# Performance work log

Measured on AMD Instinct MI355X. Metric: run time of the kernel, lower is better.

## Reference

```python
import jax, jax.numpy as jnp
import numpy as np

N_NODES = 100000
N_EDGES = 1600000
HIDDEN = 64
NUM_GRAPHS = 512


def setup_inputs() -> dict:
    key = jax.random.key(0)
    k1, k2, k3, k4, k5, k6 = jax.random.split(key, 6)
    x = jax.random.normal(k1, (N_NODES, HIDDEN), dtype=jnp.float32)
    edge_index = jax.random.randint(k2, (2, N_EDGES), 0, N_NODES, dtype=jnp.int64)
    batch = jnp.sort(jax.random.randint(k3, (N_NODES,), 0, NUM_GRAPHS, dtype=jnp.int64))
    # SAGPooling's internal GraphConv(64 -> 1): lin_rel (with bias) on aggregated
    # neighbor features, lin_root (no bias) on self features.
    s = 1.0 / np.sqrt(HIDDEN)
    W_rel = jax.random.uniform(k4, (HIDDEN, 1), dtype=jnp.float32, minval=-s, maxval=s)
    b_rel = jax.random.uniform(k5, (1,), dtype=jnp.float32, minval=-s, maxval=s)
    W_root = jax.random.uniform(k6, (HIDDEN, 1), dtype=jnp.float32, minval=-s, maxval=s)
    return {"x": x, "edge_index": edge_index, "batch": batch,
            "W_rel": W_rel, "b_rel": b_rel, "W_root": W_root}


def reference(x, edge_index, batch, W_rel, b_rel, W_root):
    n = x.shape[0]
    src, dst = edge_index[0], edge_index[1]
    # GraphConv (aggr='add'): sum x_j over in-edges, then lin_rel(aggr)+lin_root(x)
    aggr = jax.ops.segment_sum(x[src], dst, num_segments=n)          # [N, H]
    score = (aggr @ W_rel + b_rel + x @ W_root)[:, 0]                # [N]
    # min_score=-1 -> scores softmax-normalized per graph; all nodes kept in order
    m = jax.ops.segment_max(score, batch, num_segments=NUM_GRAPHS)   # [G]
    e = jnp.exp(score - m[batch])
    z = jax.ops.segment_sum(e, batch, num_segments=NUM_GRAPHS)       # [G]
    att = e / z[batch]                                               # [N]
    att_x = x * att[:, None]                                         # [N, H]
    # global_add_pool
    return jax.ops.segment_sum(att_x, batch, num_segments=NUM_GRAPHS)  # [G, H]
```

## Files before the change

kernel.cpp:

```cpp
#include <hip/hip_runtime.h>
#include <math.h>
#include <stdint.h>


#define H 64
#define TILE 4096
#define NTHR_S 1024
#define EPT (TILE / NTHR_S)
#define BUCKET_SZ 256
#define MAX_NB 400
#define CAP 5120
#define ROWS_PER_WAVE 32
#define PSCALE 16384.0f
#define INV_PSCALE 6.103515625e-05f

__global__ __launch_bounds__(256) void node_prep(
    const float4* __restrict__ x4, const float4* __restrict__ W_rel4,
    const float4* __restrict__ W_root4,
    float* __restrict__ p, float* __restrict__ r,
    float* __restrict__ num, float* __restrict__ z,
    unsigned int* __restrict__ cursor,
    int n_nodes, int num_elems, int n_graphs, int nb)
{
    int gid = (int)(blockIdx.x * blockDim.x + threadIdx.x);
    if (gid < num_elems) num[gid] = 0.0f;
    else if (gid < num_elems + n_graphs) z[gid - num_elems] = 0.0f;
    else if (gid < num_elems + n_graphs + nb)
        cursor[gid - num_elems - n_graphs] =
            (unsigned int)(gid - num_elems - n_graphs) * CAP;

    int node = blockIdx.x * 64 + (threadIdx.x >> 2);
    int q    = threadIdx.x & 3;
    if (node >= n_nodes) return;

    float pv = 0.0f, rv = 0.0f;
    #pragma unroll
    for (int kk = 0; kk < 4; ++kk) {
        float4 v  = x4[node * 16 + kk * 4 + q];
        float4 wr = W_rel4[kk * 4 + q];
        float4 wo = W_root4[kk * 4 + q];
        pv += v.x * wr.x + v.y * wr.y + v.z * wr.z + v.w * wr.w;
        rv += v.x * wo.x + v.y * wo.y + v.z * wo.z + v.w * wo.w;
    }
    pv += __shfl_xor(pv, 1, 64); pv += __shfl_xor(pv, 2, 64);
    rv += __shfl_xor(rv, 1, 64); rv += __shfl_xor(rv, 2, 64);
    if (q == 0) { p[node] = pv; r[node] = rv; }
}

__global__ __launch_bounds__(NTHR_S) void edge_sort(
    const int* __restrict__ src, const int* __restrict__ dst,
    const float* __restrict__ p,
    unsigned int* __restrict__ cursor, unsigned int* __restrict__ sorted_g,
    int n_edges, int nb)
{
    __shared__ unsigned int hist[MAX_NB];
    __shared__ unsigned int offs[MAX_NB];
    __shared__ unsigned int gbase[MAX_NB];
    __shared__ unsigned int wtot[8];
    __shared__ unsigned int svals[TILE];
    __shared__ unsigned short sbid[TILE];

    int b = blockIdx.x;
    int base = b * TILE;
    int tile_n = min(TILE, n_edges - base);
    int tid = threadIdx.x;

    if (tid < nb) hist[tid] = 0;
    __syncthreads();

    unsigned int dd[EPT]; int ss[EPT];
    float pv[EPT];
    unsigned int bk[EPT], pk[EPT], slot[EPT];

    int j0 = tid * EPT;
    if (j0 + EPT <= tile_n) {
        int4 s4 = *(const int4*)(src + base + j0);
        int4 d4 = *(const int4*)(dst + base + j0);
        ss[0] = s4.x; ss[1] = s4.y; ss[2] = s4.z; ss[3] = s4.w;
        dd[0] = (unsigned int)d4.x; dd[1] = (unsigned int)d4.y;
        dd[2] = (unsigned int)d4.z; dd[3] = (unsigned int)d4.w;
    } else {
        #pragma unroll
        for (int u = 0; u < EPT; ++u) {
            int j = j0 + u;
            if (j < tile_n) { ss[u] = src[base + j];
                              dd[u] = (unsigned int)dst[base + j]; }
            else dd[u] = 0xFFFFFFFFu;
        }
    }
    #pragma unroll
    for (int u = 0; u < EPT; ++u)
        if (dd[u] != 0xFFFFFFFFu) pv[u] = p[ss[u]];
    #pragma unroll
    for (int u = 0; u < EPT; ++u) {
        if (dd[u] != 0xFFFFFFFFu) {
            bk[u] = dd[u] >> 8;
            int q = (int)__float2int_rn(pv[u] * PSCALE);
            q = max(-8388607, min(8388607, q));
            pk[u] = ((unsigned int)q << 8) | (dd[u] & 255u);
            slot[u] = atomicAdd(&hist[bk[u]], 1u);
        }
    }
    __syncthreads();

    int wv = tid >> 6, ln = tid & 63;
    unsigned int v = 0, xs = 0;
    if (wv < 7) {
        int bin = wv * 64 + ln;
        v = (bin < nb) ? hist[bin] : 0;
        xs = v;
        #pragma unroll
        for (int off = 1; off < 64; off <<= 1) {
            unsigned int y = __shfl_up(xs, off, 64);
            if (ln >= off) xs += y;
        }
        if (ln == 63) wtot[wv] = xs;
    }
    __syncthreads();
    if (wv < 7) {
        int bin = wv * 64 + ln;
        unsigned int pre = 0;
        #pragma unroll
        for (int w2 = 0; w2 < 7; ++w2)
            pre += (w2 < wv) ? wtot[w2] : 0u;
        if (bin < nb) {
            offs[bin]  = pre + xs - v;
            gbase[bin] = v ? atomicAdd(&cursor[bin], v) : 0u;
        }
    }
    __syncthreads();

    #pragma unroll
    for (int u = 0; u < EPT; ++u) {
        if (dd[u] != 0xFFFFFFFFu) {
            unsigned int pos = offs[bk[u]] + slot[u];
            svals[pos] = pk[u];
            sbid[pos]  = (unsigned short)bk[u];
        }
    }
    __syncthreads();

    for (int j = tid; j < tile_n; j += NTHR_S) {
        unsigned int bb = sbid[j];
        unsigned int gi = gbase[bb] + ((unsigned int)j - offs[bb]);
        if (gi < (bb + 1) * (unsigned int)CAP)
            sorted_g[gi] = svals[j];
    }
}

__global__ __launch_bounds__(256) void bucket_accum(
    const unsigned int* __restrict__ sorted_g,
    const unsigned int* __restrict__ cursor,
    const float* __restrict__ r,
    float* __restrict__ e_buf, int n_nodes)
{
    __shared__ int acc[BUCKET_SZ];
    int k = blockIdx.x;
    int tid = threadIdx.x;
    acc[tid] = 0;
    __syncthreads();

    unsigned int beg = (unsigned int)k * CAP;
    unsigned int cnt = min(cursor[k] - beg, (unsigned int)CAP);
    unsigned int n4  = cnt & ~3u;
    for (unsigned int j = tid * 4; j < n4; j += 1024) {
        uint4 v = *(const uint4*)(sorted_g + beg + j);
        atomicAdd(&acc[v.x & 255u], (int)v.x >> 8);
        atomicAdd(&acc[v.y & 255u], (int)v.y >> 8);
        atomicAdd(&acc[v.z & 255u], (int)v.z >> 8);
        atomicAdd(&acc[v.w & 255u], (int)v.w >> 8);
    }
    for (unsigned int j = n4 + tid; j < cnt; j += 256) {
        unsigned int v = sorted_g[beg + j];
        atomicAdd(&acc[v & 255u], (int)v >> 8);
    }
    __syncthreads();

    int node = k * BUCKET_SZ + tid;
    if (node < n_nodes)
        e_buf[node] = __expf((float)acc[tid] * INV_PSCALE + r[node]);
}

__global__ __launch_bounds__(256) void pool(
    const float* __restrict__ x, const float* __restrict__ e_buf,
    const int* __restrict__ batch,
    float* __restrict__ num, float* __restrict__ z, int n_nodes)
{
    int wid = threadIdx.x >> 6, lane = threadIdx.x & 63;
    int row0 = (blockIdx.x * 4 + wid) * ROWS_PER_WAVE;
    if (row0 >= n_nodes) return;
    int rend = min(row0 + ROWS_PER_WAVE, n_nodes);

    int g_first = batch[row0];
    int g_last  = batch[rend - 1];

    if (g_first == g_last && rend - row0 == ROWS_PER_WAVE) {
        float acc = 0.0f, acce = 0.0f;
        #pragma unroll 8
        for (int u = 0; u < ROWS_PER_WAVE; ++u) {
            int i = row0 + u;
            float e = e_buf[i];
            acc  += x[i * H + lane] * e;
            acce += e;
        }
        unsafeAtomicAdd(&num[g_first * H + lane], acc);
        if (lane == 0) unsafeAtomicAdd(&z[g_first], acce);
        return;
    }

    int cur_g = g_first;
    float acc = 0.0f, acce = 0.0f;
    for (int i = row0; i < rend; ++i) {
        int g = batch[i];
        if (g != cur_g) {
            unsafeAtomicAdd(&num[cur_g * H + lane], acc);
            if (lane == 0) unsafeAtomicAdd(&z[cur_g], acce);
            acc = 0.0f; acce = 0.0f;
            cur_g = g;
        }
        float e = e_buf[i];
        acc  += x[i * H + lane] * e;
        acce += e;
    }
    unsafeAtomicAdd(&num[cur_g * H + lane], acc);
    if (lane == 0) unsafeAtomicAdd(&z[cur_g], acce);
}

__global__ __launch_bounds__(256) void finalize(
    const float* __restrict__ num, const float* __restrict__ z,
    float* __restrict__ out, int num_elems)
{
    int i = (int)(blockIdx.x * blockDim.x + threadIdx.x);
    if (i >= num_elems) return;
    float zz = z[i >> 6];
    out[i] = (zz != 0.0f) ? num[i] / zz : 0.0f;
}

extern "C" void kernel_launch(void* const* d_in, const int* in_sizes, int n_in,
                              void* d_out, int out_size, void* d_ws, size_t ws_size,
                              hipStream_t stream)
{
    const float* x      = (const float*)d_in[0];
    const int*   eidx   = (const int*)d_in[1];
    const int*   batch  = (const int*)d_in[2];
    const float* W_rel  = (const float*)d_in[3];
    const float* W_root = (const float*)d_in[5];
    float* out = (float*)d_out;

    const int n_nodes  = in_sizes[0] / H;
    const int n_edges  = in_sizes[1] / 2;
    const int n_graphs = out_size / H;
    const int nb     = (n_nodes + BUCKET_SZ - 1) / BUCKET_SZ;
    const int ntiles = (n_edges + TILE - 1) / TILE;

    const int* src = eidx;
    const int* dst = eidx + n_edges;

    float* p     = (float*)d_ws;
    float* r     = p + n_nodes;
    float* e_buf = r + n_nodes;
    float* z     = e_buf + n_nodes;
    float* num   = z + n_graphs;
    unsigned int* cursor = (unsigned int*)(num + out_size);
    uintptr_t raw = (uintptr_t)(cursor + nb);
    unsigned int* sorted_g = (unsigned int*)((raw + 15) & ~(uintptr_t)15);

    int np_blocks = (n_nodes + 63) / 64;
    node_prep<<<np_blocks, 256, 0, stream>>>(
        (const float4*)x, (const float4*)W_rel, (const float4*)W_root,
        p, r, num, z, cursor, n_nodes, out_size, n_graphs, nb);
    edge_sort<<<ntiles, NTHR_S, 0, stream>>>(src, dst, p, cursor, sorted_g,
                                             n_edges, nb);
    bucket_accum<<<nb, 256, 0, stream>>>(sorted_g, cursor, r, e_buf, n_nodes);
    pool<<<(n_nodes + 4 * ROWS_PER_WAVE - 1) / (4 * ROWS_PER_WAVE), 256, 0, stream>>>(
        x, e_buf, batch, num, z, n_nodes);
    finalize<<<(out_size + 255) / 256, 256, 0, stream>>>(num, z, out, out_size);
}
```

Baseline: 124.2 us.

## Fuse five kernels into one persistent cooperative kernel with grid syncs

Merges node_prep, edge_sort, bucket_accum, pool and finalize into a single cooperative kernel of 256 blocks of 1024 threads. The stages are separated by grid.sync() and each stage walks its work with grid-stride loops. This removes four kernel launch boundaries and their gaps. In exchange, every stage runs at a fixed grid size with 1024-thread blocks, which may lower occupancy and load balance: edge tiles (~391) and buckets (~391) now run on 256 blocks, and each grid barrier has its own cost.

```diff
diff --git a/kernel.cpp b/kernel.cpp
--- a/kernel.cpp
+++ b/kernel.cpp
@@ -1,239 +1,240 @@
 #include <hip/hip_runtime.h>
+#include <hip/hip_cooperative_groups.h>
 #include <math.h>
 #include <stdint.h>
 
+namespace cg = cooperative_groups;
+
 
 #define H 64
 #define TILE 4096
-#define NTHR_S 1024
-#define EPT (TILE / NTHR_S)
+#define NTHR 1024
+#define EPT (TILE / NTHR)
 #define BUCKET_SZ 256
 #define MAX_NB 400
 #define CAP 5120
-#define ROWS_PER_WAVE 32
+#define NBLK 256
 #define PSCALE 16384.0f
 #define INV_PSCALE 6.103515625e-05f
 
-__global__ __launch_bounds__(256) void node_prep(
+#define SMEM_BYTES 29408
+
+extern "C" __global__ void __launch_bounds__(NTHR) mega(
     const float4* __restrict__ x4, const float4* __restrict__ W_rel4,
     const float4* __restrict__ W_root4,
-    float* __restrict__ p, float* __restrict__ r,
-    float* __restrict__ num, float* __restrict__ z,
-    unsigned int* __restrict__ cursor,
-    int n_nodes, int num_elems, int n_graphs, int nb)
+    const int* __restrict__ src, const int* __restrict__ dst,
+    const int* __restrict__ batch, const float* __restrict__ x,
+    float* __restrict__ p, float* __restrict__ r, float* __restrict__ e_buf,
+    float* __restrict__ z, float* __restrict__ num,
+    unsigned int* __restrict__ cursor, unsigned int* __restrict__ sorted_g,
+    float* __restrict__ out,
+    int n_nodes, int n_edges, int n_graphs, int nb, int ntiles, int out_elems)
 {
-    int gid = (int)(blockIdx.x * blockDim.x + threadIdx.x);
-    if (gid < num_elems) num[gid] = 0.0f;
-    else if (gid < num_elems + n_graphs) z[gid - num_elems] = 0.0f;
-    else if (gid < num_elems + n_graphs + nb)
-        cursor[gid - num_elems - n_graphs] =
-            (unsigned int)(gid - num_elems - n_graphs) * CAP;
-
-    int node = blockIdx.x * 64 + (threadIdx.x >> 2);
-    int q    = threadIdx.x & 3;
-    if (node >= n_nodes) return;
-
-    float pv = 0.0f, rv = 0.0f;
-    #pragma unroll
-    for (int kk = 0; kk < 4; ++kk) {
-        float4 v  = x4[node * 16 + kk * 4 + q];
-        float4 wr = W_rel4[kk * 4 + q];
-        float4 wo = W_root4[kk * 4 + q];
-        pv += v.x * wr.x + v.y * wr.y + v.z * wr.z + v.w * wr.w;
-        rv += v.x * wo.x + v.y * wo.y + v.z * wo.z + v.w * wo.w;
-    }
-    pv += __shfl_xor(pv, 1, 64); pv += __shfl_xor(pv, 2, 64);
-    rv += __shfl_xor(rv, 1, 64); rv += __shfl_xor(rv, 2, 64);
-    if (q == 0) { p[node] = pv; r[node] = rv; }
-}
-
-__global__ __launch_bounds__(NTHR_S) void edge_sort(
-    const int* __restrict__ src, const int* __restrict__ dst,
-    const float* __restrict__ p,
-    unsigned int* __restrict__ cursor, unsigned int* __restrict__ sorted_g,
-    int n_edges, int nb)
-{
-    __shared__ unsigned int hist[MAX_NB];
-    __shared__ unsigned int offs[MAX_NB];
-    __shared__ unsigned int gbase[MAX_NB];
-    __shared__ unsigned int wtot[8];
-    __shared__ unsigned int svals[TILE];
-    __shared__ unsigned short sbid[TILE];
-
-    int b = blockIdx.x;
-    int base = b * TILE;
-    int tile_n = min(TILE, n_edges - base);
-    int tid = threadIdx.x;
-
-    if (tid < nb) hist[tid] = 0;
-    __syncthreads();
-
-    unsigned int dd[EPT]; int ss[EPT];
-    float pv[EPT];
-    unsigned int bk[EPT], pk[EPT], slot[EPT];
-
-    int j0 = tid * EPT;
-    if (j0 + EPT <= tile_n) {
-        int4 s4 = *(const int4*)(src + base + j0);
-        int4 d4 = *(const int4*)(dst + base + j0);
-        ss[0] = s4.x; ss[1] = s4.y; ss[2] = s4.z; ss[3] = s4.w;
-        dd[0] = (unsigned int)d4.x; dd[1] = (unsigned int)d4.y;
-        dd[2] = (unsigned int)d4.z; dd[3] = (unsigned int)d4.w;
-    } else {
+    __shared__ __align__(16) char smem[SMEM_BYTES];
+    unsigned int*  hist  = (unsigned int*)(smem);
+    unsigned int*  offs  = (unsigned int*)(smem + 1600);
+    unsigned int*  gbase = (unsigned int*)(smem + 3200);
+    unsigned int*  wtot  = (unsigned int*)(smem + 4800);
+    unsigned int*  svals = (unsigned int*)(smem + 4832);
+    unsigned short* sbid = (unsigned short*)(smem + 21216);
+    int* acc = (int*)(smem);
+
+    cg::grid_group grid = cg::this_grid();
+    const int tid  = threadIdx.x;
+    const int gtid = blockIdx.x * NTHR + tid;
+    const int T    = gridDim.x * NTHR;
+
+    for (int i = gtid; i < out_elems + n_graphs + nb; i += T) {
+        if (i < out_elems) num[i] = 0.0f;
+        else if (i < out_elems + n_graphs) z[i - out_elems] = 0.0f;
+        else cursor[i - out_elems - n_graphs] =
+                 (unsigned int)(i - out_elems - n_graphs) * CAP;
+    }
+    {
+        int q = gtid & 3;
+        for (int node = gtid >> 2; node < n_nodes; node += T >> 2) {
+            float pv = 0.0f, rv = 0.0f;
+            #pragma unroll
+            for (int kk = 0; kk < 4; ++kk) {
+                float4 v  = x4[node * 16 + kk * 4 + q];
+                float4 wr = W_rel4[kk * 4 + q];
+                float4 wo = W_root4[kk * 4 + q];
+                pv += v.x * wr.x + v.y * wr.y + v.z * wr.z + v.w * wr.w;
+                rv += v.x * wo.x + v.y * wo.y + v.z * wo.z + v.w * wo.w;
+            }
+            pv += __shfl_xor(pv, 1, 64); pv += __shfl_xor(pv, 2, 64);
+            rv += __shfl_xor(rv, 1, 64); rv += __shfl_xor(rv, 2, 64);
+            if (q == 0) { p[node] = pv; r[node] = rv; }
+        }
+    }
+    grid.sync();
+
+    for (int t = blockIdx.x; t < ntiles; t += gridDim.x) {
+        int base = t * TILE;
+        int tile_n = min(TILE, n_edges - base);
+
+        if (tid < nb) hist[tid] = 0;
+        __syncthreads();
+
+        unsigned int dd[EPT]; int ss[EPT];
+        float pv[EPT];
+        unsigned int bk[EPT], pk[EPT], slot[EPT];
+
+        int j0 = tid * EPT;
+        if (j0 + EPT <= tile_n) {
+            int4 s4 = *(const int4*)(src + base + j0);
+            int4 d4 = *(const int4*)(dst + base + j0);
+            ss[0] = s4.x; ss[1] = s4.y; ss[2] = s4.z; ss[3] = s4.w;
+            dd[0] = (unsigned int)d4.x; dd[1] = (unsigned int)d4.y;
+            dd[2] = (unsigned int)d4.z; dd[3] = (unsigned int)d4.w;
+        } else {
+            #pragma unroll
+            for (int u = 0; u < EPT; ++u) {
+                int j = j0 + u;
+                if (j < tile_n) { ss[u] = src[base + j];
+                                  dd[u] = (unsigned int)dst[base + j]; }
+                else dd[u] = 0xFFFFFFFFu;
+            }
+        }
+        #pragma unroll
+        for (int u = 0; u < EPT; ++u)
+            if (dd[u] != 0xFFFFFFFFu) pv[u] = p[ss[u]];
         #pragma unroll
         for (int u = 0; u < EPT; ++u) {
-            int j = j0 + u;
-            if (j < tile_n) { ss[u] = src[base + j];
-                              dd[u] = (unsigned int)dst[base + j]; }
-            else dd[u] = 0xFFFFFFFFu;
-        }
-    }
-    #pragma unroll
-    for (int u = 0; u < EPT; ++u)
-        if (dd[u] != 0xFFFFFFFFu) pv[u] = p[ss[u]];
-    #pragma unroll
-    for (int u = 0; u < EPT; ++u) {
-        if (dd[u] != 0xFFFFFFFFu) {
-            bk[u] = dd[u] >> 8;
-            int q = (int)__float2int_rn(pv[u] * PSCALE);
-            q = max(-8388607, min(8388607, q));
-            pk[u] = ((unsigned int)q << 8) | (dd[u] & 255u);
-            slot[u] = atomicAdd(&hist[bk[u]], 1u);
-        }
-    }
-    __syncthreads();
-
-    int wv = tid >> 6, ln = tid & 63;
-    unsigned int v = 0, xs = 0;
-    if (wv < 7) {
-        int bin = wv * 64 + ln;
-        v = (bin < nb) ? hist[bin] : 0;
-        xs = v;
+            if (dd[u] != 0xFFFFFFFFu) {
+                bk[u] = dd[u] >> 8;
+                int q = (int)__float2int_rn(pv[u] * PSCALE);
+                q = max(-8388607, min(8388607, q));
+                pk[u] = ((unsigned int)q << 8) | (dd[u] & 255u);
+                slot[u] = atomicAdd(&hist[bk[u]], 1u);
+            }
+        }
+        __syncthreads();
+
+        int wv = tid >> 6, ln = tid & 63;
+        unsigned int v = 0, xs = 0;
+        if (wv < 7) {
+            int bin = wv * 64 + ln;
+            v = (bin < nb) ? hist[bin] : 0;
+            xs = v;
+            #pragma unroll
+            for (int off = 1; off < 64; off <<= 1) {
+                unsigned int y = __shfl_up(xs, off, 64);
+                if (ln >= off) xs += y;
+            }
+            if (ln == 63) wtot[wv] = xs;
+        }
+        __syncthreads();
+        if (wv < 7) {
+            int bin = wv * 64 + ln;
+            unsigned int pre = 0;
+            #pragma unroll
+            for (int w2 = 0; w2 < 7; ++w2)
+                pre += (w2 < wv) ? wtot[w2] : 0u;
+            if (bin < nb) {
+                offs[bin]  = pre + xs - v;
+                gbase[bin] = v ? atomicAdd(&cursor[bin], v) : 0u;
+            }
+        }
+        __syncthreads();
+
         #pragma unroll
-        for (int off = 1; off < 64; off <<= 1) {
-            unsigned int y = __shfl_up(xs, off, 64);
-            if (ln >= off) xs += y;
-        }
-        if (ln == 63) wtot[wv] = xs;
-    }
-    __syncthreads();
-    if (wv < 7) {
-        int bin = wv * 64 + ln;
-        unsigned int pre = 0;
-        #pragma unroll
-        for (int w2 = 0; w2 < 7; ++w2)
-            pre += (w2 < wv) ? wtot[w2] : 0u;
-        if (bin < nb) {
-            offs[bin]  = pre + xs - v;
-            gbase[bin] = v ? atomicAdd(&cursor[bin], v) : 0u;
-        }
-    }
-    __syncthreads();
-
-    #pragma unroll
-    for (int u = 0; u < EPT; ++u) {
-        if (dd[u] != 0xFFFFFFFFu) {
-            unsigned int pos = offs[bk[u]] + slot[u];
-            svals[pos] = pk[u];
-            sbid[pos]  = (unsigned short)bk[u];
-        }
-    }
-    __syncthreads();
-
-    for (int j = tid; j < tile_n; j += NTHR_S) {
-        unsigned int bb = sbid[j];
-        unsigned int gi = gbase[bb] + ((unsigned int)j - offs[bb]);
-        if (gi < (bb + 1) * (unsigned int)CAP)
-            sorted_g[gi] = svals[j];
-    }
-}
-
-__global__ __launch_bounds__(256) void bucket_accum(
-    const unsigned int* __restrict__ sorted_g,
-    const unsigned int* __restrict__ cursor,
-    const float* __restrict__ r,
-    float* __restrict__ e_buf, int n_nodes)
-{
-    __shared__ int acc[BUCKET_SZ];
-    int k = blockIdx.x;
-    int tid = threadIdx.x;
-    acc[tid] = 0;
-    __syncthreads();
-
-    unsigned int beg = (unsigned int)k * CAP;
-    unsigned int cnt = min(cursor[k] - beg, (unsigned int)CAP);
-    unsigned int n4  = cnt & ~3u;
-    for (unsigned int j = tid * 4; j < n4; j += 1024) {
-        uint4 v = *(const uint4*)(sorted_g + beg + j);
-        atomicAdd(&acc[v.x & 255u], (int)v.x >> 8);
-        atomicAdd(&acc[v.y & 255u], (int)v.y >> 8);
-        atomicAdd(&acc[v.z & 255u], (int)v.z >> 8);
-        atomicAdd(&acc[v.w & 255u], (int)v.w >> 8);
-    }
-    for (unsigned int j = n4 + tid; j < cnt; j += 256) {
-        unsigned int v = sorted_g[beg + j];
-        atomicAdd(&acc[v & 255u], (int)v >> 8);
-    }
-    __syncthreads();
-
-    int node = k * BUCKET_SZ + tid;
-    if (node < n_nodes)
-        e_buf[node] = __expf((float)acc[tid] * INV_PSCALE + r[node]);
-}
-
-__global__ __launch_bounds__(256) void pool(
-    const float* __restrict__ x, const float* __restrict__ e_buf,
-    const int* __restrict__ batch,
-    float* __restrict__ num, float* __restrict__ z, int n_nodes)
-{
-    int wid = threadIdx.x >> 6, lane = threadIdx.x & 63;
-    int row0 = (blockIdx.x * 4 + wid) * ROWS_PER_WAVE;
-    if (row0 >= n_nodes) return;
-    int rend = min(row0 + ROWS_PER_WAVE, n_nodes);
-
-    int g_first = batch[row0];
-    int g_last  = batch[rend - 1];
-
-    if (g_first == g_last && rend - row0 == ROWS_PER_WAVE) {
-        float acc = 0.0f, acce = 0.0f;
-        #pragma unroll 8
-        for (int u = 0; u < ROWS_PER_WAVE; ++u) {
-            int i = row0 + u;
-            float e = e_buf[i];
-            acc  += x[i * H + lane] * e;
-            acce += e;
-        }
-        unsafeAtomicAdd(&num[g_first * H + lane], acc);
-        if (lane == 0) unsafeAtomicAdd(&z[g_first], acce);
-        return;
-    }
-
-    int cur_g = g_first;
-    float acc = 0.0f, acce = 0.0f;
-    for (int i = row0; i < rend; ++i) {
-        int g = batch[i];
-        if (g != cur_g) {
-            unsafeAtomicAdd(&num[cur_g * H + lane], acc);
-            if (lane == 0) unsafeAtomicAdd(&z[cur_g], acce);
-            acc = 0.0f; acce = 0.0f;
-            cur_g = g;
-        }
-        float e = e_buf[i];
-        acc  += x[i * H + lane] * e;
-        acce += e;
-    }
-    unsafeAtomicAdd(&num[cur_g * H + lane], acc);
-    if (lane == 0) unsafeAtomicAdd(&z[cur_g], acce);
-}
-
-__global__ __launch_bounds__(256) void finalize(
-    const float* __restrict__ num, const float* __restrict__ z,
-    float* __restrict__ out, int num_elems)
-{
-    int i = (int)(blockIdx.x * blockDim.x + threadIdx.x);
-    if (i >= num_elems) return;
-    float zz = z[i >> 6];
-    out[i] = (zz != 0.0f) ? num[i] / zz : 0.0f;
+        for (int u = 0; u < EPT; ++u) {
+            if (dd[u] != 0xFFFFFFFFu) {
+                unsigned int pos = offs[bk[u]] + slot[u];
+                svals[pos] = pk[u];
+                sbid[pos]  = (unsigned short)bk[u];
+            }
+        }
+        __syncthreads();
+
+        for (int j = tid; j < tile_n; j += NTHR) {
+            unsigned int bb = sbid[j];
+            unsigned int gi = gbase[bb] + ((unsigned int)j - offs[bb]);
+            if (gi < (bb + 1) * (unsigned int)CAP)
+                sorted_g[gi] = svals[j];
+        }
+        __syncthreads();
+    }
+    grid.sync();
+
+    for (int k = blockIdx.x; k < nb; k += gridDim.x) {
+        if (tid < BUCKET_SZ) acc[tid] = 0;
+        __syncthreads();
+
+        unsigned int beg = (unsigned int)k * CAP;
+        unsigned int cnt = min(cursor[k] - beg, (unsigned int)CAP);
+        unsigned int n4  = cnt & ~3u;
+        for (unsigned int j = tid * 4; j < n4; j += NTHR * 4) {
+            uint4 vv = *(const uint4*)(sorted_g + beg + j);
+            atomicAdd(&acc[vv.x & 255u], (int)vv.x >> 8);
+            atomicAdd(&acc[vv.y & 255u], (int)vv.y >> 8);
+            atomicAdd(&acc[vv.z & 255u], (int)vv.z >> 8);
+            atomicAdd(&acc[vv.w & 255u], (int)vv.w >> 8);
+        }
+        for (unsigned int j = n4 + tid; j < cnt; j += NTHR) {
+            unsigned int vv = sorted_g[beg + j];
+            atomicAdd(&acc[vv & 255u], (int)vv >> 8);
+        }
+        __syncthreads();
+
+        if (tid < BUCKET_SZ) {
+            int node = k * BUCKET_SZ + tid;
+            if (node < n_nodes)
+                e_buf[node] = __expf((float)acc[tid] * INV_PSCALE + r[node]);
+        }
+        __syncthreads();
+    }
+    grid.sync();
+
+    {
+        int lane = tid & 63;
+        int wave = blockIdx.x * (NTHR / 64) + (tid >> 6);
+        int nwin = (n_nodes + 31) / 32;
+        int wstride = gridDim.x * (NTHR / 64);
+        for (int w = wave; w < nwin; w += wstride) {
+            int row0 = w * 32;
+            int rend = min(row0 + 32, n_nodes);
+            int g_first = batch[row0];
+            int g_last  = batch[rend - 1];
+
+            if (g_first == g_last && rend - row0 == 32) {
+                float a = 0.0f, ae = 0.0f;
+                #pragma unroll 8
+                for (int u = 0; u < 32; ++u) {
+                    int i = row0 + u;
+                    float e = e_buf[i];
+                    a  += x[i * H + lane] * e;
+                    ae += e;
+                }
+                unsafeAtomicAdd(&num[g_first * H + lane], a);
+                if (lane == 0) unsafeAtomicAdd(&z[g_first], ae);
+            } else {
+                int cur_g = g_first;
+                float a = 0.0f, ae = 0.0f;
+                for (int i = row0; i < rend; ++i) {
+                    int g = batch[i];
+                    if (g != cur_g) {
+                        unsafeAtomicAdd(&num[cur_g * H + lane], a);
+                        if (lane == 0) unsafeAtomicAdd(&z[cur_g], ae);
+                        a = 0.0f; ae = 0.0f;
+                        cur_g = g;
+                    }
+                    float e = e_buf[i];
+                    a  += x[i * H + lane] * e;
+                    ae += e;
+                }
+                unsafeAtomicAdd(&num[cur_g * H + lane], a);
+                if (lane == 0) unsafeAtomicAdd(&z[cur_g], ae);
+            }
+        }
+    }
+    grid.sync();
+
+    for (int i = gtid; i < out_elems; i += T) {
+        float zz = z[i >> 6];
+        out[i] = (zz != 0.0f) ? num[i] / zz : 0.0f;
+    }
 }
 
 extern "C" void kernel_launch(void* const* d_in, const int* in_sizes, int n_in,
@@ -247,11 +248,12 @@
     const float* W_root = (const float*)d_in[5];
     float* out = (float*)d_out;
 
-    const int n_nodes  = in_sizes[0] / H;
-    const int n_edges  = in_sizes[1] / 2;
-    const int n_graphs = out_size / H;
-    const int nb     = (n_nodes + BUCKET_SZ - 1) / BUCKET_SZ;
-    const int ntiles = (n_edges + TILE - 1) / TILE;
+    int n_nodes  = in_sizes[0] / H;
+    int n_edges  = in_sizes[1] / 2;
+    int n_graphs = out_size / H;
+    int nb     = (n_nodes + BUCKET_SZ - 1) / BUCKET_SZ;
+    int ntiles = (n_edges + TILE - 1) / TILE;
+    int out_elems = out_size;
 
     const int* src = eidx;
     const int* dst = eidx + n_edges;
@@ -265,14 +267,18 @@
     uintptr_t raw = (uintptr_t)(cursor + nb);
     unsigned int* sorted_g = (unsigned int*)((raw + 15) & ~(uintptr_t)15);
 
-    int np_blocks = (n_nodes + 63) / 64;
-    node_prep<<<np_blocks, 256, 0, stream>>>(
-        (const float4*)x, (const float4*)W_rel, (const float4*)W_root,
-        p, r, num, z, cursor, n_nodes, out_size, n_graphs, nb);
-    edge_sort<<<ntiles, NTHR_S, 0, stream>>>(src, dst, p, cursor, sorted_g,
-                                             n_edges, nb);
-    bucket_accum<<<nb, 256, 0, stream>>>(sorted_g, cursor, r, e_buf, n_nodes);
-    pool<<<(n_nodes + 4 * ROWS_PER_WAVE - 1) / (4 * ROWS_PER_WAVE), 256, 0, stream>>>(
-        x, e_buf, batch, num, z, n_nodes);
-    finalize<<<(out_size + 255) / 256, 256, 0, stream>>>(num, z, out, out_size);
+    const float4* x4  = (const float4*)x;
+    const float4* wr4 = (const float4*)W_rel;
+    const float4* wo4 = (const float4*)W_root;
+
+    void* args[] = {
+        (void*)&x4, (void*)&wr4, (void*)&wo4,
+        (void*)&src, (void*)&dst, (void*)&batch, (void*)&x,
+        (void*)&p, (void*)&r, (void*)&e_buf, (void*)&z, (void*)&num,
+        (void*)&cursor, (void*)&sorted_g, (void*)&out,
+        (void*)&n_nodes, (void*)&n_edges, (void*)&n_graphs,
+        (void*)&nb, (void*)&ntiles, (void*)&out_elems,
+    };
+    hipLaunchCooperativeKernel((const void*)mega, dim3(NBLK), dim3(NTHR),
+                               args, 0, stream);
 }
```

New measurement: 258.9 us. 108% more time.
